# Kernel optimization log

Measured on AMD Instinct MI355X. Metric: run time of the kernel, lower is better.

## Reference

```python
import jax, jax.numpy as jnp
import numpy as np

D = 128; N_CELLS = 512; N_GENES = 256; HEADS = 4; HD = D // HEADS
E_SP = 8192; E_GRN = 2048

def _ln(x, g, b):
    m = jnp.mean(x, -1, keepdims=True)
    v = jnp.var(x, -1, keepdims=True)
    return (x - m) * jax.lax.rsqrt(v + 1e-5) * g + b

def setup_inputs():
    key = jax.random.key(0)
    ks = jax.random.split(key, 16)
    w = lambda i, shp: jax.random.normal(ks[i], shp, jnp.float32) * 0.02
    return {
        "high_emb": jax.random.normal(ks[0], (N_CELLS, D), jnp.float32),
        "low_emb": jax.random.normal(ks[1], (N_CELLS, N_GENES, D), jnp.float32),
        "spatial_edge_index": jax.random.randint(ks[2], (2, E_SP), 0, N_CELLS),
        "grn_edge_index": jax.random.randint(ks[3], (2, E_GRN), 0, N_GENES),
        "gin_w1": w(4, (D, 2 * D)), "gin_b1": jnp.zeros((2 * D,)),
        "gin_w2": w(5, (2 * D, D)), "gin_b2": jnp.zeros((D,)),
        "gin_eps": jnp.zeros(()),
        "gin_ln_g": jnp.ones((D,)), "gin_ln_b": jnp.zeros((D,)),
        "tc_wq": w(6, (D, D)), "tc_bq": jnp.zeros((D,)),
        "tc_wk": w(7, (D, D)), "tc_bk": jnp.zeros((D,)),
        "tc_wv": w(8, (D, D)), "tc_bv": jnp.zeros((D,)),
        "tc_wskip": w(9, (D, D)), "tc_bskip": jnp.zeros((D,)),
        "tc_ln_g": jnp.ones((D,)), "tc_ln_b": jnp.zeros((D,)),
        "cross_w": w(10, (6, D, D)), "cross_b": jnp.zeros((6, D)),
        "agg_w": w(11, (D, D)), "agg_b": jnp.zeros((D,)),
        "nh_g": jnp.ones((D,)), "nh_b": jnp.zeros((D,)),
        "nl_g": jnp.ones((D,)), "nl_b": jnp.zeros((D,)),
    }

def _forward(high_emb, low_emb, spatial_edge_index, grn_edge_index,
             gin_w1, gin_b1, gin_w2, gin_b2, gin_eps, gin_ln_g, gin_ln_b,
             tc_wq, tc_bq, tc_wk, tc_bk, tc_wv, tc_bv, tc_wskip, tc_bskip,
             tc_ln_g, tc_ln_b, cross_w, cross_b, agg_w, agg_b,
             nh_g, nh_b, nl_g, nl_b):
    # ---- high level: GIN conv over spatial cell graph ----
    s_src, s_dst = spatial_edge_index[0], spatial_edge_index[1]
    agg = jax.ops.segment_sum(high_emb[s_src], s_dst, num_segments=N_CELLS)
    h = (1.0 + gin_eps) * high_emb + agg
    h = jax.nn.gelu(h @ gin_w1 + gin_b1, approximate=False) @ gin_w2 + gin_b2
    high_out = _ln(h, gin_ln_g, gin_ln_b)

    # ---- low level: TransformerConv on per-cell GRN (edge structure shared across cells) ----
    g_src, g_dst = grn_edge_index[0], grn_edge_index[1]
    q = (low_emb @ tc_wq + tc_bq).reshape(N_CELLS, N_GENES, HEADS, HD)
    k = (low_emb @ tc_wk + tc_bk).reshape(N_CELLS, N_GENES, HEADS, HD)
    v = (low_emb @ tc_wv + tc_bv).reshape(N_CELLS, N_GENES, HEADS, HD)
    # per-edge attention logits, edge axis leading for segment ops: (E, C, H)
    logits = jnp.einsum('cehd,cehd->ech', q[:, g_dst], k[:, g_src]) / np.sqrt(HD).astype(np.float32)
    mx = jax.lax.stop_gradient(jax.ops.segment_max(logits, g_dst, num_segments=N_GENES))
    ex = jnp.exp(logits - mx[g_dst])
    den = jax.ops.segment_sum(ex, g_dst, num_segments=N_GENES)
    alpha = ex / den[g_dst]                          # (E, C, H) softmax per target gene
    v_s = jnp.moveaxis(v[:, g_src], 0, 1)            # (E, C, H, HD)
    out = jax.ops.segment_sum(alpha[..., None] * v_s, g_dst, num_segments=N_GENES)
    out = jnp.moveaxis(out, 0, 1).reshape(N_CELLS, N_GENES, D)
    out = out + low_emb @ tc_wskip + tc_bskip        # PyG root_weight skip
    low_out = _ln(out, tc_ln_g, tc_ln_b)

    # ---- gene aggregation + cross-level sigmoid gating ----
    gene_agg = jax.nn.gelu(jnp.mean(low_out, axis=1) @ agg_w + agg_b, approximate=False)
    scale = D ** -0.5
    q1 = high_out @ cross_w[0] + cross_b[0]
    k1 = gene_agg @ cross_w[1] + cross_b[1]
    v1 = gene_agg @ cross_w[2] + cross_b[2]
    high_cross = jax.nn.sigmoid(jnp.sum(q1 * k1, -1, keepdims=True) * scale) * v1
    q2 = gene_agg @ cross_w[3] + cross_b[3]
    k2 = high_out @ cross_w[4] + cross_b[4]
    v2 = high_out @ cross_w[5] + cross_b[5]
    low_cross = jax.nn.sigmoid(jnp.sum(q2 * k2, -1, keepdims=True) * scale) * v2

    high_new = _ln(high_emb + high_out + high_cross, nh_g, nh_b)
    low_new = _ln(low_emb + low_out + low_cross[:, None, :], nl_g, nl_b)
    return (high_new, low_new)

def reference(high_emb, low_emb, spatial_edge_index, grn_edge_index,
              gin_w1, gin_b1, gin_w2, gin_b2, gin_eps, gin_ln_g, gin_ln_b,
              tc_wq, tc_bq, tc_wk, tc_bk, tc_wv, tc_bv, tc_wskip, tc_bskip,
              tc_ln_g, tc_ln_b, cross_w, cross_b, agg_w, agg_b,
              nh_g, nh_b, nl_g, nl_b):
    return _forward(high_emb, low_emb, spatial_edge_index, grn_edge_index,
                    gin_w1, gin_b1, gin_w2, gin_b2, gin_eps, gin_ln_g, gin_ln_b,
                    tc_wq, tc_bq, tc_wk, tc_bk, tc_wv, tc_bv, tc_wskip, tc_bskip,
                    tc_ln_g, tc_ln_b, cross_w, cross_b, agg_w, agg_b,
                    nh_g, nh_b, nl_g, nl_b)
```

## Files before the change

### kernel.cpp

```cpp
#include <hip/hip_runtime.h>
#include <hip/hip_bf16.h>
#include <math.h>

#define N_CELLS 512
#define N_GENES 256
#define D 128
#define HEADS 4
#define HD 32
#define E_SP 8192
#define E_GRN 2048

typedef __attribute__((ext_vector_type(8))) short bf16x8;
typedef __attribute__((ext_vector_type(4))) float f32x4;


__device__ __forceinline__ float gelu_exact(float x) {
    return 0.5f * x * (1.0f + erff(x * 0.70710678118654752f));
}

__device__ __forceinline__ unsigned short f2bf(float f) {
    unsigned u = __float_as_uint(f);
    return (unsigned short)((u + 0x7FFFu + ((u >> 16) & 1u)) >> 16);
}

template<int NT>
__device__ __forceinline__ float blockSum(float v, float* sbuf) {
    #pragma unroll
    for (int off = 32; off > 0; off >>= 1) v += __shfl_down(v, off, 64);
    int lane = threadIdx.x & 63, wid = threadIdx.x >> 6;
    __syncthreads();
    if (lane == 0) sbuf[wid] = v;
    __syncthreads();
    float r = 0.f;
    #pragma unroll
    for (int i = 0; i < NT / 64; ++i) r += sbuf[i];
    return r;
}


__global__ __launch_bounds__(512) void sp_csr_kernel(const int* __restrict__ sp,
                                                     int* __restrict__ sp_off,
                                                     int* __restrict__ sp_src) {
    __shared__ int cnt[512];
    __shared__ int scan[512];
    __shared__ int cur[512];
    int t = threadIdx.x;
    cnt[t] = 0;
    __syncthreads();
    for (int e = t; e < E_SP; e += 512) atomicAdd(&cnt[sp[E_SP + e]], 1);
    __syncthreads();
    scan[t] = cnt[t];
    __syncthreads();
    #pragma unroll
    for (int s = 1; s < 512; s <<= 1) {
        int v = (t >= s) ? scan[t - s] : 0;
        __syncthreads();
        scan[t] += v;
        __syncthreads();
    }
    int excl = scan[t] - cnt[t];
    sp_off[t] = excl;
    if (t == 511) sp_off[512] = scan[511];
    cur[t] = excl;
    __syncthreads();
    for (int e = t; e < E_SP; e += 512) {
        int dst = sp[E_SP + e];
        int pos = atomicAdd(&cur[dst], 1);
        sp_src[pos] = sp[e];
    }
}


__global__ void cnt_build_kernel(const int* __restrict__ grn, unsigned* __restrict__ cnt4) {
    int e = blockIdx.x * 256 + threadIdx.x;
    int src = grn[e], dst = grn[E_GRN + e];
    atomicAdd(&cnt4[dst * 32 + (src >> 3)], 1u << (4 * (src & 7)));
}


__global__ __launch_bounds__(256) void gin_mlp_kernel(
    const float* __restrict__ high,
    const int* __restrict__ sp_off, const int* __restrict__ sp_src,
    const float* __restrict__ eps,
    const float* __restrict__ w1, const float* __restrict__ b1,
    const float* __restrict__ w2, const float* __restrict__ b2,
    const float* __restrict__ lng, const float* __restrict__ lnb,
    float* __restrict__ high_out) {
    int c = blockIdx.x;
    int t = threadIdx.x;
    __shared__ float h[D];
    __shared__ float h1[2 * D];
    __shared__ float sbuf[4];
    if (t < D) {
        float acc = 0.f;
        int off = sp_off[c], end = sp_off[c + 1];
        for (int i = off; i < end; ++i) acc += high[(size_t)sp_src[i] * D + t];
        h[t] = (1.f + eps[0]) * high[c * D + t] + acc;
    }
    __syncthreads();
    float a = b1[t];
    for (int k = 0; k < D; ++k) a += h[k] * w1[k * 256 + t];
    h1[t] = gelu_exact(a);
    __syncthreads();
    float x = 0.f;
    if (t < D) {
        float a2 = b2[t];
        for (int k = 0; k < 256; ++k) a2 += h1[k] * w2[k * D + t];
        x = a2;
    }
    float s = blockSum<256>(x, sbuf);
    float mean = s * (1.f / 128.f);
    float xm = (t < D) ? (x - mean) : 0.f;
    float var = blockSum<256>(xm * xm, sbuf) * (1.f / 128.f);
    if (t < D) high_out[c * D + t] = xm * rsqrtf(var + 1e-5f) * lng[t] + lnb[t];
}


__global__ __launch_bounds__(256) void wt_kernel(
    const float* __restrict__ wq, const float* __restrict__ wk,
    const float* __restrict__ wv, const float* __restrict__ wskip,
    unsigned short* __restrict__ wt4) {
    __shared__ float tile[128][132];
    int w = blockIdx.x;
    const float* Wp = (w == 0) ? wq : (w == 1) ? wk : (w == 2) ? wv : wskip;
    int t = threadIdx.x;
    #pragma unroll
    for (int rep = 0; rep < 16; ++rep) {
        int f4 = rep * 256 + t;
        float4 v = ((const float4*)Wp)[f4];
        int f = f4 * 4;
        int k = f >> 7, n = f & 127;
        tile[k][n] = v.x; tile[k][n + 1] = v.y; tile[k][n + 2] = v.z; tile[k][n + 3] = v.w;
    }
    __syncthreads();
    unsigned short* out = wt4 + (size_t)w * 16384;
    #pragma unroll
    for (int rep = 0; rep < 16; ++rep) {
        int f4 = rep * 256 + t;
        int f = f4 * 4;
        int n = f >> 7, k = f & 127;
        ushort4 o;
        o.x = f2bf(tile[k][n]);
        o.y = f2bf(tile[k + 1][n]);
        o.z = f2bf(tile[k + 2][n]);
        o.w = f2bf(tile[k + 3][n]);
        *(ushort4*)(out + (size_t)n * 128 + k) = o;
    }
}


__global__ __launch_bounds__(256, 2) void proj4_kernel(
    const float* __restrict__ X,
    const unsigned short* __restrict__ Wt4,
    const float* __restrict__ bq, const float* __restrict__ bk,
    const float* __restrict__ bv, const float* __restrict__ bs,
    unsigned short* __restrict__ Yq, unsigned short* __restrict__ Yk,
    unsigned short* __restrict__ Yv, float* __restrict__ Yskip) {
    __shared__ short Xs[128 * 128];
    __shared__ short Ws[128 * 128];
    int t = threadIdx.x;
    int lane = t & 63, wid = t >> 6;
    const float* Xblk = X + (size_t)blockIdx.x * 128 * 128;

    #pragma unroll
    for (int rep = 0; rep < 16; ++rep) {
        int f4 = rep * 256 + t;
        float4 xv = ((const float4*)Xblk)[f4];
        int f = f4 * 4;
        int row = f >> 7, k = f & 127;
        unsigned p0 = (unsigned)f2bf(xv.x) | ((unsigned)f2bf(xv.y) << 16);
        unsigned p1 = (unsigned)f2bf(xv.z) | ((unsigned)f2bf(xv.w) << 16);
        int eidx = (row * 128 + k) ^ ((row & 7) << 3);
        *(uint2*)(&Xs[eidx]) = make_uint2(p0, p1);
    }

    const float* Bs_[4] = {bq, bk, bv, bs};
    int lr = lane & 15, lg = lane >> 4;
    int rbase = (wid >> 1) * 64, cbase = (wid & 1) * 64;
    int orow0 = blockIdx.x * 128 + rbase;

    for (int w = 0; w < 4; ++w) {
        __syncthreads();
        const uint2* Wsrc = (const uint2*)(Wt4 + (size_t)w * 16384);
        #pragma unroll
        for (int rep = 0; rep < 16; ++rep) {
            int e4 = rep * 256 + t;
            uint2 d2 = Wsrc[e4];
            int f = e4 * 4;
            int n = f >> 7, k = f & 127;
            *(uint2*)(&Ws[(n * 128 + k) ^ ((n & 7) << 3)]) = d2;
        }
        __syncthreads();

        f32x4 acc[4][4] = {};
        #pragma unroll
        for (int ks = 0; ks < 4; ++ks) {
            int k0 = ks * 32 + lg * 8;
            bf16x8 a[4], b[4];
            #pragma unroll
            for (int m = 0; m < 4; ++m) {
                int row = rbase + m * 16 + lr;
                a[m] = *(const bf16x8*)(&Xs[(row * 128 + k0) ^ ((row & 7) << 3)]);
            }
            #pragma unroll
            for (int n = 0; n < 4; ++n) {
                int col = cbase + n * 16 + lr;
                b[n] = *(const bf16x8*)(&Ws[(col * 128 + k0) ^ ((col & 7) << 3)]);
            }
            #pragma unroll
            for (int m = 0; m < 4; ++m)
                #pragma unroll
                for (int n = 0; n < 4; ++n)
                    acc[m][n] = __builtin_amdgcn_mfma_f32_16x16x32_bf16(a[m], b[n], acc[m][n], 0, 0, 0);
        }

        const float* Bb = Bs_[w];
        if (w < 3) {
            unsigned short* Y = (w == 0) ? Yq : (w == 1) ? Yk : Yv;
            #pragma unroll
            for (int n = 0; n < 4; ++n) {
                int col = cbase + n * 16 + lr;
                float bias = Bb[col];
                #pragma unroll
                for (int m = 0; m < 4; ++m)
                    #pragma unroll
                    for (int j = 0; j < 4; ++j) {
                        int row = orow0 + m * 16 + lg * 4 + j;
                        Y[(size_t)row * 128 + col] = f2bf(acc[m][n][j] + bias);
                    }
            }
        } else {
            #pragma unroll
            for (int n = 0; n < 4; ++n) {
                int col = cbase + n * 16 + lr;
                float bias = Bb[col];
                #pragma unroll
                for (int m = 0; m < 4; ++m)
                    #pragma unroll
                    for (int j = 0; j < 4; ++j) {
                        int row = orow0 + m * 16 + lg * 4 + j;
                        Yskip[(size_t)row * 128 + col] = acc[m][n][j] + bias;
                    }
            }
        }
    }
}


__global__ __launch_bounds__(256) void vt_kernel(const unsigned short* __restrict__ v,
                                                 unsigned short* __restrict__ vt) {
    __shared__ unsigned short tile[128][130];
    int c = blockIdx.x;
    size_t cb = (size_t)c * 32768;
    int t = threadIdx.x;
    for (int half = 0; half < 2; ++half) {
        __syncthreads();
        const unsigned* src = (const unsigned*)(v + cb + (size_t)half * 16384);
        #pragma unroll
        for (int i = 0; i < 32; ++i) {
            int f2 = i * 256 + t;
            unsigned u = src[f2];
            int g = f2 >> 6, d2 = f2 & 63;
            *(unsigned*)&tile[g][2 * d2] = u;
        }
        __syncthreads();
        #pragma unroll
        for (int i = 0; i < 32; ++i) {
            int f2 = i * 256 + t;
            int d = f2 >> 6, gp = f2 & 63;
            unsigned u = (unsigned)tile[2 * gp][d] | ((unsigned)tile[2 * gp + 1][d] << 16);
            ((unsigned*)(vt + cb + (size_t)d * 256 + half * 128))[gp] = u;
        }
    }
}


__global__ __launch_bounds__(256, 2) void attn_dense_kernel(
    const unsigned short* __restrict__ q, const unsigned short* __restrict__ k,
    const unsigned short* __restrict__ vt,
    const unsigned* __restrict__ cnt4,
    const float* __restrict__ lng, const float* __restrict__ lnb,
    float* __restrict__ outp) {
    extern __shared__ char smem[];
    unsigned* cntL = (unsigned*)smem;
    unsigned short* Pl = (unsigned short*)(smem + 32768);
    float* obuf = (float*)(smem + 65536);
    int c = blockIdx.x;
    int t = threadIdx.x;
    int lane = t & 63, h = t >> 6;
    int lr = lane & 15, lg = lane >> 4;
    size_t cb = (size_t)c * 32768;

    #pragma unroll
    for (int i = 0; i < 32; ++i) {
        int idx = i * 256 + t;
        unsigned w = cnt4[idx];
        int dst = idx >> 5, w8 = idx & 31;
        cntL[dst * 32 + (w8 ^ (dst & 31))] = w;
    }

    bf16x8 kf[16];
    #pragma unroll
    for (int n = 0; n < 16; ++n)
        kf[n] = *(const bf16x8*)(k + cb + (size_t)(n * 16 + lr) * 128 + h * 32 + lg * 8);
    bf16x8 vf[2][8];
    #pragma unroll
    for (int ht = 0; ht < 2; ++ht)
        #pragma unroll
        for (int m = 0; m < 8; ++m)
            vf[ht][m] = *(const bf16x8*)(vt + cb + (size_t)(h * 32 + ht * 16 + lr) * 256 + m * 32 + lg * 8);

    __syncthreads();

    unsigned short* Pw = Pl + h * 4096;
    const float scale = 0.17677669529663687f;

    for (int tile = 0; tile < 16; ++tile) {
        bf16x8 qf = *(const bf16x8*)(q + cb + (size_t)(tile * 16 + lr) * 128 + h * 32 + lg * 8);

        f32x4 s[16];
        const f32x4 z = {0.f, 0.f, 0.f, 0.f};
        #pragma unroll
        for (int n = 0; n < 16; ++n)
            s[n] = __builtin_amdgcn_mfma_f32_16x16x32_bf16(kf[n], qf, z, 0, 0, 0);

        int dst = tile * 16 + lr;
        unsigned cw[16];
        float m = -1e30f;
        #pragma unroll
        for (int n = 0; n < 16; ++n) {
            int w8 = 2 * n + (lg >> 1);
            unsigned w = cntL[dst * 32 + (w8 ^ (dst & 31))];
            cw[n] = (w >> (16 * (lg & 1))) & 0xFFFFu;
            #pragma unroll
            for (int j = 0; j < 4; ++j) {
                float val = s[n][j] * scale;
                s[n][j] = val;
                if ((cw[n] >> (4 * j)) & 15) m = fmaxf(m, val);
            }
        }
        m = fmaxf(m, __shfl_xor(m, 16));
        m = fmaxf(m, __shfl_xor(m, 32));
        float den = 0.f;
        #pragma unroll
        for (int n = 0; n < 16; ++n) {
            #pragma unroll
            for (int j = 0; j < 4; ++j) {
                int cnt = (cw[n] >> (4 * j)) & 15;
                float e = cnt ? (float)cnt * expf(s[n][j] - m) : 0.f;
                s[n][j] = e;
                den += e;
            }
        }
        den += __shfl_xor(den, 16);
        den += __shfl_xor(den, 32);
        float inv = den > 0.f ? 1.f / den : 0.f;
        #pragma unroll
        for (int n = 0; n < 16; ++n) {
            unsigned lo = (unsigned)f2bf(s[n][0] * inv) | ((unsigned)f2bf(s[n][1] * inv) << 16);
            unsigned hi = (unsigned)f2bf(s[n][2] * inv) | ((unsigned)f2bf(s[n][3] * inv) << 16);
            int e = (16 * n + 4 * lg) ^ (8 * (lr & 7));
            *(uint2*)(Pw + lr * 256 + e) = make_uint2(lo, hi);
        }
        f32x4 o[2] = {};
        #pragma unroll
        for (int m2 = 0; m2 < 8; ++m2) {
            int e = (32 * m2 + 8 * lg) ^ (8 * (lr & 7));
            bf16x8 pf = *(const bf16x8*)(Pw + lr * 256 + e);
            o[0] = __builtin_amdgcn_mfma_f32_16x16x32_bf16(vf[0][m2], pf, o[0], 0, 0, 0);
            o[1] = __builtin_amdgcn_mfma_f32_16x16x32_bf16(vf[1][m2], pf, o[1], 0, 0, 0);
        }
        #pragma unroll
        for (int ht = 0; ht < 2; ++ht)
            #pragma unroll
            for (int j = 0; j < 4; ++j) {
                int d = h * 32 + ht * 16 + lg * 4 + j;
                obuf[lr * 128 + (d ^ (4 * (lr & 7)))] = o[ht][j];
            }
        __syncthreads();

        {
            int gl = t >> 4, sub = t & 15;
            int g = tile * 16 + gl;
            int swz = 4 * (gl & 7);
            float4 oa = *(float4*)(obuf + gl * 128 + ((sub * 8) ^ swz));
            float4 ob = *(float4*)(obuf + gl * 128 + ((sub * 8 + 4) ^ swz));
            const float* skp = outp + cb + (size_t)g * 128 + sub * 8;
            float4 sa = *(const float4*)(skp);
            float4 sb = *(const float4*)(skp + 4);
            float x[8] = {oa.x + sa.x, oa.y + sa.y, oa.z + sa.z, oa.w + sa.w,
                          ob.x + sb.x, ob.y + sb.y, ob.z + sb.z, ob.w + sb.w};
            float sm = 0.f;
            #pragma unroll
            for (int i = 0; i < 8; ++i) sm += x[i];
            sm += __shfl_xor(sm, 1); sm += __shfl_xor(sm, 2);
            sm += __shfl_xor(sm, 4); sm += __shfl_xor(sm, 8);
            float mean = sm * (1.f / 128.f);
            float vv = 0.f;
            #pragma unroll
            for (int i = 0; i < 8; ++i) { x[i] -= mean; vv += x[i] * x[i]; }
            vv += __shfl_xor(vv, 1); vv += __shfl_xor(vv, 2);
            vv += __shfl_xor(vv, 4); vv += __shfl_xor(vv, 8);
            float rs = rsqrtf(vv * (1.f / 128.f) + 1e-5f);
            float4 ga = *(const float4*)(lng + sub * 8);
            float4 gb = *(const float4*)(lng + sub * 8 + 4);
            float4 ba = *(const float4*)(lnb + sub * 8);
            float4 bb = *(const float4*)(lnb + sub * 8 + 4);
            float* op = outp + cb + (size_t)g * 128 + sub * 8;
            float4 r1 = {x[0] * rs * ga.x + ba.x, x[1] * rs * ga.y + ba.y,
                         x[2] * rs * ga.z + ba.z, x[3] * rs * ga.w + ba.w};
            float4 r2 = {x[4] * rs * gb.x + bb.x, x[5] * rs * gb.y + bb.y,
                         x[6] * rs * gb.z + bb.z, x[7] * rs * gb.w + bb.w};
            *(float4*)(op) = r1;
            *(float4*)(op + 4) = r2;
        }
        __syncthreads();
    }
}


__global__ __launch_bounds__(128) void gene_agg_kernel(
    const float* __restrict__ low_out,
    const float* __restrict__ agg_w, const float* __restrict__ agg_b,
    float* __restrict__ gene_agg) {
    int c = blockIdx.x, d = threadIdx.x;
    const float* base = low_out + (size_t)c * N_GENES * D;
    float s = 0.f;
    for (int g = 0; g < N_GENES; ++g) s += base[g * D + d];
    __shared__ float m[D];
    m[d] = s * (1.f / 256.f);
    __syncthreads();
    float acc = agg_b[d];
    for (int k = 0; k < D; ++k) acc += m[k] * agg_w[k * D + d];
    gene_agg[c * D + d] = gelu_exact(acc);
}


__global__ __launch_bounds__(128) void cross_kernel(
    const float* __restrict__ high_emb, const float* __restrict__ high_out,
    const float* __restrict__ gene_agg,
    const float* __restrict__ cw, const float* __restrict__ cb,
    const float* __restrict__ nhg, const float* __restrict__ nhb,
    float* __restrict__ high_new, float* __restrict__ low_cross) {
    int c = blockIdx.x, d = threadIdx.x;
    __shared__ float ho[D], ga[D];
    __shared__ float sbuf[2];
    ho[d] = high_out[c * D + d];
    ga[d] = gene_agg[c * D + d];
    __syncthreads();
    float q1 = cb[0 * D + d], k1 = cb[1 * D + d], v1 = cb[2 * D + d];
    float q2 = cb[3 * D + d], k2 = cb[4 * D + d], v2 = cb[5 * D + d];
    for (int k = 0; k < D; ++k) {
        float hv = ho[k], gv = ga[k];
        q1 += hv * cw[0 * 16384 + k * D + d];
        k1 += gv * cw[1 * 16384 + k * D + d];
        v1 += gv * cw[2 * 16384 + k * D + d];
        q2 += gv * cw[3 * 16384 + k * D + d];
        k2 += hv * cw[4 * 16384 + k * D + d];
        v2 += hv * cw[5 * 16384 + k * D + d];
    }
    const float scale = 0.08838834764831845f;
    float s1 = blockSum<128>(q1 * k1, sbuf);
    float s2 = blockSum<128>(q2 * k2, sbuf);
    float hc = (1.f / (1.f + expf(-s1 * scale))) * v1;
    float lc = (1.f / (1.f + expf(-s2 * scale))) * v2;
    low_cross[c * D + d] = lc;
    float x = high_emb[c * D + d] + ho[d] + hc;
    float sm = blockSum<128>(x, sbuf);
    float mean = sm * (1.f / 128.f);
    float xm = x - mean;
    float var = blockSum<128>(xm * xm, sbuf) * (1.f / 128.f);
    high_new[c * D + d] = xm * rsqrtf(var + 1e-5f) * nhg[d] + nhb[d];
}


__global__ __launch_bounds__(128) void low_final_kernel(
    const float* __restrict__ low_emb, const float* __restrict__ low_cross,
    const float* __restrict__ nlg, const float* __restrict__ nlb,
    float* __restrict__ out) {
    int cg = blockIdx.x;
    int c = cg >> 8;
    int d = threadIdx.x;
    size_t idx = (size_t)cg * D + d;
    float x = low_emb[idx] + out[idx] + low_cross[c * D + d];
    __shared__ float sbuf[2];
    float s = blockSum<128>(x, sbuf);
    float mean = s * (1.f / 128.f);
    float xm = x - mean;
    float var = blockSum<128>(xm * xm, sbuf) * (1.f / 128.f);
    out[idx] = xm * rsqrtf(var + 1e-5f) * nlg[d] + nlb[d];
}


extern "C" void kernel_launch(void* const* d_in, const int* in_sizes, int n_in,
                              void* d_out, int out_size, void* d_ws, size_t ws_size,
                              hipStream_t stream) {
    const float* high_emb = (const float*)d_in[0];
    const float* low_emb  = (const float*)d_in[1];
    const int*   sp       = (const int*)d_in[2];
    const int*   grn      = (const int*)d_in[3];
    const float* gin_w1   = (const float*)d_in[4];
    const float* gin_b1   = (const float*)d_in[5];
    const float* gin_w2   = (const float*)d_in[6];
    const float* gin_b2   = (const float*)d_in[7];
    const float* gin_eps  = (const float*)d_in[8];
    const float* gin_lng  = (const float*)d_in[9];
    const float* gin_lnb  = (const float*)d_in[10];
    const float* tc_wq    = (const float*)d_in[11];
    const float* tc_bq    = (const float*)d_in[12];
    const float* tc_wk    = (const float*)d_in[13];
    const float* tc_bk    = (const float*)d_in[14];
    const float* tc_wv    = (const float*)d_in[15];
    const float* tc_bv    = (const float*)d_in[16];
    const float* tc_wskip = (const float*)d_in[17];
    const float* tc_bskip = (const float*)d_in[18];
    const float* tc_lng   = (const float*)d_in[19];
    const float* tc_lnb   = (const float*)d_in[20];
    const float* cross_w  = (const float*)d_in[21];
    const float* cross_b  = (const float*)d_in[22];
    const float* agg_w    = (const float*)d_in[23];
    const float* agg_b    = (const float*)d_in[24];
    const float* nh_g     = (const float*)d_in[25];
    const float* nh_b     = (const float*)d_in[26];
    const float* nl_g     = (const float*)d_in[27];
    const float* nl_b     = (const float*)d_in[28];

    float* out = (float*)d_out;
    float* out_high = out;
    float* out_low  = out + N_CELLS * D;

    const size_t LOW_N = (size_t)N_CELLS * N_GENES * D;

    unsigned short* q_b = (unsigned short*)d_ws;
    unsigned short* k_b = q_b + LOW_N;
    unsigned short* v_b = k_b + LOW_N;
    unsigned short* vt_b = v_b + LOW_N;
    float* ws_high_out  = (float*)(vt_b + LOW_N);
    float* ws_gene_agg  = ws_high_out + N_CELLS * D;
    float* ws_low_cross = ws_gene_agg + N_CELLS * D;
    unsigned short* wt4 = (unsigned short*)(ws_low_cross + N_CELLS * D);
    unsigned* cnt4 = (unsigned*)(wt4 + 4 * 128 * 128);
    int* sp_off  = (int*)(cnt4 + 8192);
    int* sp_src  = sp_off + 516;

    sp_csr_kernel<<<1, 512, 0, stream>>>(sp, sp_off, sp_src);
    hipMemsetAsync(cnt4, 0, 8192 * sizeof(unsigned), stream);
    cnt_build_kernel<<<E_GRN / 256, 256, 0, stream>>>(grn, cnt4);
    wt_kernel<<<4, 256, 0, stream>>>(tc_wq, tc_wk, tc_wv, tc_wskip, wt4);

    gin_mlp_kernel<<<N_CELLS, 256, 0, stream>>>(high_emb, sp_off, sp_src, gin_eps,
        gin_w1, gin_b1, gin_w2, gin_b2, gin_lng, gin_lnb, ws_high_out);

    proj4_kernel<<<N_CELLS * N_GENES / 128, 256, 0, stream>>>(
        low_emb, wt4, tc_bq, tc_bk, tc_bv, tc_bskip, q_b, k_b, v_b, out_low);

    vt_kernel<<<N_CELLS, 256, 0, stream>>>(v_b, vt_b);

    attn_dense_kernel<<<N_CELLS, 256, 73728, stream>>>(
        q_b, k_b, vt_b, cnt4, tc_lng, tc_lnb, out_low);

    gene_agg_kernel<<<N_CELLS, 128, 0, stream>>>(out_low, agg_w, agg_b, ws_gene_agg);

    cross_kernel<<<N_CELLS, 128, 0, stream>>>(high_emb, ws_high_out, ws_gene_agg,
        cross_w, cross_b, nh_g, nh_b, out_high, ws_low_cross);

    low_final_kernel<<<N_CELLS * N_GENES, 128, 0, stream>>>(
        low_emb, ws_low_cross, nl_g, nl_b, out_low);
}
```

Before: 616.4 us.

## Stage K in LDS and stream V from global in attention kernel

Moves the per-cell K matrix from per-thread registers into a swizzled 64KB LDS region, and reads V fragments from global memory inside the tile loop instead of preloading them into registers. The skip-connection load for the layernorm is hoisted to the start of each tile so its latency overlaps the MFMA work. Register pressure drops, but LDS grows to 136KB, launch bounds fall to one block per CU, and V is re-read from global (or cache) on all 16 tiles.

```diff
diff --git a/kernel.cpp b/kernel.cpp
--- a/kernel.cpp
+++ b/kernel.cpp
@@ -275,54 +275,62 @@
 }
 
 
-__global__ __launch_bounds__(256, 2) void attn_dense_kernel(
+__global__ __launch_bounds__(256, 1) void attn_dense_kernel(
     const unsigned short* __restrict__ q, const unsigned short* __restrict__ k,
     const unsigned short* __restrict__ vt,
     const unsigned* __restrict__ cnt4,
     const float* __restrict__ lng, const float* __restrict__ lnb,
     float* __restrict__ outp) {
     extern __shared__ char smem[];
-    unsigned* cntL = (unsigned*)smem;
-    unsigned short* Pl = (unsigned short*)(smem + 32768);
-    float* obuf = (float*)(smem + 65536);
+    unsigned* cntL = (unsigned*)(smem + 65536);
+    unsigned short* Pl = (unsigned short*)(smem + 98304);
+    float* obuf = (float*)(smem + 131072);
     int c = blockIdx.x;
     int t = threadIdx.x;
     int lane = t & 63, h = t >> 6;
     int lr = lane & 15, lg = lane >> 4;
+    int gl = t >> 4, sub = t & 15;
     size_t cb = (size_t)c * 32768;
 
+    {
+        const uint4* src = (const uint4*)(k + cb);
+        #pragma unroll
+        for (int i = 0; i < 16; ++i) {
+            int f4 = i * 256 + t;
+            uint4 d = src[f4];
+            int row = f4 >> 4, c16 = f4 & 15;
+            *(uint4*)(smem + row * 256 + ((c16 * 16) ^ ((row & 7) << 4))) = d;
+        }
+    }
     #pragma unroll
     for (int i = 0; i < 32; ++i) {
         int idx = i * 256 + t;
         unsigned w = cnt4[idx];
-        int dst = idx >> 5, w8 = idx & 31;
-        cntL[dst * 32 + (w8 ^ (dst & 31))] = w;
-    }
-
-    bf16x8 kf[16];
-    #pragma unroll
-    for (int n = 0; n < 16; ++n)
-        kf[n] = *(const bf16x8*)(k + cb + (size_t)(n * 16 + lr) * 128 + h * 32 + lg * 8);
-    bf16x8 vf[2][8];
-    #pragma unroll
-    for (int ht = 0; ht < 2; ++ht)
-        #pragma unroll
-        for (int m = 0; m < 8; ++m)
-            vf[ht][m] = *(const bf16x8*)(vt + cb + (size_t)(h * 32 + ht * 16 + lr) * 256 + m * 32 + lg * 8);
-
+        int dst2 = idx >> 5, w8 = idx & 31;
+        cntL[dst2 * 32 + (w8 ^ (dst2 & 31))] = w;
+    }
     __syncthreads();
 
     unsigned short* Pw = Pl + h * 4096;
     const float scale = 0.17677669529663687f;
+    int kcol = h * 64 + lg * 16;
+    int kswz = (lr & 7) << 4;
 
     for (int tile = 0; tile < 16; ++tile) {
+        const float* skp = outp + cb + (size_t)(tile * 16 + gl) * 128 + sub * 8;
+        float4 sa = *(const float4*)(skp);
+        float4 sb = *(const float4*)(skp + 4);
+
         bf16x8 qf = *(const bf16x8*)(q + cb + (size_t)(tile * 16 + lr) * 128 + h * 32 + lg * 8);
 
         f32x4 s[16];
         const f32x4 z = {0.f, 0.f, 0.f, 0.f};
         #pragma unroll
-        for (int n = 0; n < 16; ++n)
-            s[n] = __builtin_amdgcn_mfma_f32_16x16x32_bf16(kf[n], qf, z, 0, 0, 0);
+        for (int n = 0; n < 16; ++n) {
+            int row = n * 16 + lr;
+            bf16x8 kf = *(const bf16x8*)(smem + row * 256 + (kcol ^ kswz));
+            s[n] = __builtin_amdgcn_mfma_f32_16x16x32_bf16(kf, qf, z, 0, 0, 0);
+        }
 
         int dst = tile * 16 + lr;
         unsigned cw[16];
@@ -367,8 +375,10 @@
         for (int m2 = 0; m2 < 8; ++m2) {
             int e = (32 * m2 + 8 * lg) ^ (8 * (lr & 7));
             bf16x8 pf = *(const bf16x8*)(Pw + lr * 256 + e);
-            o[0] = __builtin_amdgcn_mfma_f32_16x16x32_bf16(vf[0][m2], pf, o[0], 0, 0, 0);
-            o[1] = __builtin_amdgcn_mfma_f32_16x16x32_bf16(vf[1][m2], pf, o[1], 0, 0, 0);
+            bf16x8 v0 = *(const bf16x8*)(vt + cb + (size_t)(h * 32 + lr) * 256 + m2 * 32 + lg * 8);
+            bf16x8 v1 = *(const bf16x8*)(vt + cb + (size_t)(h * 32 + 16 + lr) * 256 + m2 * 32 + lg * 8);
+            o[0] = __builtin_amdgcn_mfma_f32_16x16x32_bf16(v0, pf, o[0], 0, 0, 0);
+            o[1] = __builtin_amdgcn_mfma_f32_16x16x32_bf16(v1, pf, o[1], 0, 0, 0);
         }
         #pragma unroll
         for (int ht = 0; ht < 2; ++ht)
@@ -380,14 +390,10 @@
         __syncthreads();
 
         {
-            int gl = t >> 4, sub = t & 15;
             int g = tile * 16 + gl;
             int swz = 4 * (gl & 7);
             float4 oa = *(float4*)(obuf + gl * 128 + ((sub * 8) ^ swz));
             float4 ob = *(float4*)(obuf + gl * 128 + ((sub * 8 + 4) ^ swz));
-            const float* skp = outp + cb + (size_t)g * 128 + sub * 8;
-            float4 sa = *(const float4*)(skp);
-            float4 sb = *(const float4*)(skp + 4);
             float x[8] = {oa.x + sa.x, oa.y + sa.y, oa.z + sa.z, oa.w + sa.w,
                           ob.x + sb.x, ob.y + sb.y, ob.z + sb.z, ob.w + sb.w};
             float sm = 0.f;
@@ -556,7 +562,7 @@
 
     vt_kernel<<<N_CELLS, 256, 0, stream>>>(v_b, vt_b);
 
-    attn_dense_kernel<<<N_CELLS, 256, 73728, stream>>>(
+    attn_dense_kernel<<<N_CELLS, 256, 139264, stream>>>(
         q_b, k_b, vt_b, cnt4, tc_lng, tc_lnb, out_low);
 
     gene_agg_kernel<<<N_CELLS, 128, 0, stream>>>(out_low, agg_w, agg_b, ws_gene_agg);
```

Measured after the change: 561.8 us. -8.9%, faster.
